# Kernel tuning notes

Hardware: AMD Instinct MI355X
Metric: run time of the kernel (lower is better)

## Reference

```python
import jax, jax.numpy as jnp
import numpy as np

SPATIAL = [(56, 100), (28, 50), (14, 25), (7, 13)]
L_TOT = sum(h * w for h, w in SPATIAL)  # 7441
IMG_H, IMG_W = 448.0, 800.0
HH, NLEV, NPTS = 8, 4, 4
C, FFN = 256, 1024
PC = [-54.0, -54.0, -5.0, 54.0, 54.0, 3.0]
GRID_XY = 1080 // 8


def mlp2(x, w1, b1, w2, b2):
    return jnp.maximum(x @ w1 + b1, 0.0) @ w2 + b2


def ln(x):
    m = x.mean(-1, keepdims=True)
    v = ((x - m) ** 2).mean(-1, keepdims=True)
    return (x - m) * jax.lax.rsqrt(v + 1e-5)


def bilinear_sample(feat, loc):
    # feat [h,w,D]; loc [N,2] normalized to [0,1]; zero padding, align_corners=False
    h, w = feat.shape[0], feat.shape[1]
    x = loc[:, 0] * w - 0.5
    y = loc[:, 1] * h - 0.5
    x0f = jnp.floor(x); y0f = jnp.floor(y)
    wx = (x - x0f)[:, None]; wy = (y - y0f)[:, None]
    x0 = x0f.astype(jnp.int32); y0 = y0f.astype(jnp.int32)
    def g(xi, yi):
        inb = ((xi >= 0) & (xi < w) & (yi >= 0) & (yi < h))[:, None]
        return feat[jnp.clip(yi, 0, h - 1), jnp.clip(xi, 0, w - 1)] * inb
    return (g(x0, y0) * (1 - wx) * (1 - wy) + g(x0 + 1, y0) * wx * (1 - wy)
            + g(x0, y0 + 1) * (1 - wx) * wy + g(x0 + 1, y0 + 1) * wx * wy)


def setup_inputs() -> dict:
    key = jax.random.key(0)
    ks = jax.random.split(key, 40)
    B, V, P = 4, 6, 200
    f = jnp.float32
    def w(i, shape, s=0.05):
        return jax.random.normal(ks[i], shape, f) * s
    inp = {
        'img_query_feat': jax.random.normal(ks[1], (B, C, P), f),
        'img_query_pos': jax.random.uniform(ks[2], (B, P, 3), dtype=f),
        'img_query_view_mask': jax.random.randint(ks[3], (B, P, V), 0, 2).astype(jnp.int32),
        'img_feats_stack': jax.random.normal(ks[4], (B, V, C, L_TOT), f),
        'normal_img_feats_pos_stack': jax.random.normal(ks[5], (L_TOT, 2), f),
        'lidar2img_rt': jnp.eye(4, dtype=f) + 0.01 * jax.random.normal(ks[0], (B, V, 4, 4), f),
        'lidar2cam_r': jnp.broadcast_to(jnp.eye(3, dtype=f), (B, V, 3, 3)) + 0.01 * jax.random.normal(ks[6], (B, V, 3, 3), f),
        'lidar2cam_t': jax.random.normal(ks[7], (B, V, 3), f),
        'qpos_w1': w(8, (3, C)), 'qpos_b1': jnp.zeros((C,), f),
        'qpos_w2': w(9, (C, C)), 'qpos_b2': jnp.zeros((C,), f),
        'kpos_w1': w(10, (6, C)), 'kpos_b1': jnp.zeros((C,), f),
        'kpos_w2': w(11, (C, C)), 'kpos_b2': jnp.zeros((C,), f),
        'sa_wq': w(12, (C, C)), 'sa_wk': w(13, (C, C)),
        'sa_wv': w(14, (C, C)), 'sa_wo': w(15, (C, C)),
        'dv_w': w(16, (C, C)),
        'doff_w': w(17, (C, HH * NLEV * NPTS * 2)), 'doff_b': jnp.zeros((HH * NLEV * NPTS * 2,), f),
        'dattn_w': w(18, (C, HH * NLEV * NPTS)), 'dattn_b': jnp.zeros((HH * NLEV * NPTS,), f),
        'dout_w': w(19, (C, C)),
        'ffn_w1': w(20, (C, FFN)), 'ffn_b1': jnp.zeros((FFN,), f),
        'ffn_w2': w(21, (FFN, C)), 'ffn_b2': jnp.zeros((C,), f),
        'pred_w1': w(22, (C, C)), 'pred_b1': jnp.zeros((C,), f),
        'pred_w2': w(23, (C, 3)), 'pred_b2': jnp.zeros((3,), f),
    }
    return inp


def reference(img_query_feat, img_query_pos, img_query_view_mask, img_feats_stack,
              normal_img_feats_pos_stack, lidar2img_rt, lidar2cam_r, lidar2cam_t,
              qpos_w1, qpos_b1, qpos_w2, qpos_b2, kpos_w1, kpos_b1, kpos_w2, kpos_b2,
              sa_wq, sa_wk, sa_wv, sa_wo, dv_w, doff_w, doff_b, dattn_w, dattn_b, dout_w,
              ffn_w1, ffn_b1, ffn_w2, ffn_b2, pred_w1, pred_b1, pred_w2, pred_b2):
    B, V, _, L = img_feats_stack.shape
    P = img_query_feat.shape[-1]
    Dh = C // HH

    # key 3D positions: denormalize -> backproject via inv(lidar2img) -> append cam center
    pos2d = jax.nn.sigmoid(normal_img_feats_pos_stack) * jnp.array([IMG_W, IMG_H], jnp.float32)
    pos4 = jnp.concatenate([pos2d, jnp.ones((L, 2), pos2d.dtype)], -1)  # [L,4]
    inv_rt = jnp.linalg.inv(lidar2img_rt)                               # [B,V,4,4]
    key3d = jnp.einsum('bvij,lj->bvli', inv_rt, pos4)[..., :3]          # [B,V,L,3]
    cam_t = -jnp.einsum('bvji,bvj->bvi', lidar2cam_r, lidar2cam_t)      # [B,V,3]
    key_pos6 = jnp.concatenate([key3d, jnp.broadcast_to(cam_t[:, :, None], key3d.shape)], -1)
    kpos_emb = mlp2(key_pos6, kpos_w1, kpos_b1, kpos_w2, kpos_b2)       # [B,V,L,C]
    qpos_emb = mlp2(img_query_pos, qpos_w1, qpos_b1, qpos_w2, qpos_b2)  # [B,P,C]

    # per-view normalized reference points from lidar->image projection
    qpad = jnp.concatenate([img_query_pos, jnp.ones((B, P, 1), img_query_pos.dtype)], -1)
    proj = jnp.einsum('bvij,bpj->bvpi', lidar2img_rt, qpad)
    ref = (proj[..., :2] / proj[..., 2:3]) / jnp.array([IMG_W, IMG_H], jnp.float32)  # [B,V,P,2]

    # on-image mask; views with <=1 query are skipped (as in original)
    mv = jnp.transpose(img_query_view_mask > 0, (0, 2, 1))  # [B,V,P]
    mv = mv & (mv.sum(-1, keepdims=True) > 1)

    # self attention among on-image queries (shared qkv, per-view key mask)
    x = jnp.transpose(img_query_feat, (0, 2, 1))  # [B,P,C]
    xq = x + qpos_emb
    q = (xq @ sa_wq).reshape(B, P, HH, Dh)
    k = (xq @ sa_wk).reshape(B, P, HH, Dh)
    v = (x @ sa_wv).reshape(B, P, HH, Dh)
    logits = jnp.einsum('bqhd,bkhd->bhqk', q, k) / np.sqrt(Dh).astype(np.float32)
    logits = logits[:, None] + jnp.where(mv[:, :, None, None, :], 0.0, -1e9)  # [B,V,HH,P,P]
    attn = jax.nn.softmax(logits, axis=-1)
    sa = jnp.einsum('bvhqk,bkhd->bvqhd', attn, v).reshape(B, V, P, C) @ sa_wo
    x1 = ln(x[:, None] + sa)  # [B,V,P,C]

    # multi-scale deformable cross attention
    vals = ((jnp.transpose(img_feats_stack, (0, 1, 3, 2)) + kpos_emb) @ dv_w).reshape(B, V, L, HH, Dh)
    q2 = x1 + qpos_emb[:, None]
    off = (q2 @ doff_w + doff_b).reshape(B, V, P, HH, NLEV, NPTS, 2)
    aw = jax.nn.softmax((q2 @ dattn_w + dattn_b).reshape(B, V, P, HH, NLEV * NPTS), -1)
    aw = aw.reshape(B, V, P, HH, NLEV, NPTS)
    wh = jnp.array([[float(w_), float(h_)] for (h_, w_) in SPATIAL], jnp.float32)  # [NLEV,2]
    loc = ref[:, :, :, None, None, None, :] + off / wh[:, None, :]
    out = jnp.zeros((B, V, P, HH, Dh), x.dtype)
    start = 0
    for l, (h_, w_) in enumerate(SPATIAL):
        feat_l = vals[:, :, start:start + h_ * w_]
        start += h_ * w_
        feat_l = jnp.transpose(feat_l.reshape(B, V, h_, w_, HH, Dh), (0, 1, 4, 2, 3, 5)).reshape(B * V * HH, h_, w_, Dh)
        loc_l = jnp.transpose(loc[:, :, :, :, l], (0, 1, 3, 2, 4, 5)).reshape(B * V * HH, P * NPTS, 2)
        s = jax.vmap(bilinear_sample)(feat_l, loc_l).reshape(B, V, HH, P, NPTS, Dh)
        out = out + jnp.einsum('bvhpnd,bvphn->bvphd', s, aw[:, :, :, :, l])
    x2 = ln(x1 + out.reshape(B, V, P, C) @ dout_w)
    x3 = ln(x2 + mlp2(x2, ffn_w1, ffn_b1, ffn_w2, ffn_b2))  # [B,V,P,C]

    # masked scatter-accumulate across views, count-normalized
    mk = mv[..., None].astype(x.dtype)            # [B,V,P,1]
    fused = (x3 * mk).sum(1) / (mk.sum(1) + 1e-4)  # [B,P,C]
    img_query_feat_out = jnp.transpose(fused, (0, 2, 1))

    # prediction head: center refinement + BEV normalization
    center = mlp2(fused, pred_w1, pred_b1, pred_w2, pred_b2) + img_query_pos  # [B,P,3]
    img_query_pos_out = jax.lax.stop_gradient(center)
    cx = (center[..., 0] - PC[0]) / (PC[3] - PC[0]) * GRID_XY
    cy = (center[..., 1] - PC[1]) / (PC[4] - PC[1]) * GRID_XY
    center_bev = jnp.stack([cx, cy], -1)
    img_query_pos_bev = jax.lax.stop_gradient(center_bev)
    height = jnp.transpose(center[..., 2:3], (0, 2, 1))
    center_out = jnp.transpose(center_bev, (0, 2, 1))
    return img_query_feat_out, img_query_pos_out, img_query_pos_bev, center_out, height
```

## Files before the change

### kernel.cpp

```cpp
#include <hip/hip_runtime.h>
#include <hip/hip_bf16.h>
#include <cstdint>
#include <cstddef>

using bf16 = __hip_bfloat16;
#define DEVFN static __device__ __forceinline__

constexpr int B = 4, V = 6, P = 200, C = 256, HH = 8, Dh = 32, NLEV = 4, NPTS = 4, FFN = 1024;
constexpr int L = 7441;
constexpr int BV = B * V, BP = B * P, BVP = B * V * P, BVL = B * V * L;
constexpr float IMG_W = 800.f, IMG_H = 448.f;

__constant__ int cLH[4] = {56, 28, 14, 7};
__constant__ int cLW[4] = {100, 50, 25, 13};
__constant__ int cLS[4] = {0, 5600, 7000, 7350};

constexpr size_t IRT   = 0;
constexpr size_t CAMT  = IRT + (size_t)BV * 16;
constexpr size_t MFLAG = CAMT + (size_t)BV * 3;
constexpr size_t Xo    = MFLAG + BV;
constexpr size_t QPOSo = Xo + (size_t)BP * C;
constexpr size_t Qo    = QPOSo + (size_t)BP * C;
constexpr size_t Ko    = Qo + (size_t)BP * C;
constexpr size_t VVo   = Ko + (size_t)BP * C;
constexpr size_t LOGo  = VVo + (size_t)BP * C;
constexpr size_t SAo   = LOGo + (size_t)B * HH * P * P;
constexpr size_t X1o   = SAo + (size_t)BVP * C;
constexpr size_t REFo  = X1o + (size_t)BVP * C;
constexpr size_t OFFo  = REFo + (size_t)BVP * 2;
constexpr size_t AWo   = OFFo + (size_t)BVP * 256;
constexpr size_t OUTSo = AWo + (size_t)BVP * 128;
constexpr size_t X2o   = OUTSo + (size_t)BVP * C;
constexpr size_t X3o   = X2o + (size_t)BVP * C;
constexpr size_t FUSEDo= X3o + (size_t)BVP * C;
constexpr size_t WS_FLOATS = FUSEDo + (size_t)BP * C;
constexpr size_t VALS_BYTE_OFF = ((WS_FLOATS * 4 + 255) / 256) * 256;
constexpr size_t VALS_ELEMS = (size_t)BVL * C;

constexpr size_t KW2T_O  = 0;
constexpr size_t DVWT_O  = 65536;
constexpr size_t WOT_O   = 131072;
constexpr size_t DOUTT_O = 196608;
constexpr size_t OAWT_O  = 262144;
constexpr size_t QKVT_O  = 360448;
constexpr size_t W1T_O   = 753664;
constexpr size_t W2T_O   = 1015808;
constexpr size_t HIDB_O  = 1277952;

constexpr size_t O0 = 0;
constexpr size_t O1 = O0 + (size_t)B * C * P;
constexpr size_t O2 = O1 + (size_t)B * P * 3;
constexpr size_t O3 = O2 + (size_t)B * P * 2;
constexpr size_t O4 = O3 + (size_t)B * 2 * P;

DEVFN float tof(bf16 x) { return __bfloat162float(x); }
DEVFN bf16  tobf(float x) { return __float2bfloat16(x); }

typedef __attribute__((ext_vector_type(8))) short short8;
typedef __attribute__((ext_vector_type(4))) float floatx4;

DEVFN float blockReduceSum(float v, float* red) {
    int j = threadIdx.x;
    __syncthreads();
    red[j] = v; __syncthreads();
    for (int s = 128; s > 0; s >>= 1) { if (j < s) red[j] += red[j + s]; __syncthreads(); }
    return red[0];
}

DEVFN float dotK(const float* __restrict__ s, const float* __restrict__ W, int j, int N, int K) {
    float acc = 0.f;
    for (int k = 0; k < K; k += 4) {
        float4 h = *(const float4*)(s + k);
        acc += h.x * W[(size_t)(k + 0) * N + j];
        acc += h.y * W[(size_t)(k + 1) * N + j];
        acc += h.z * W[(size_t)(k + 2) * N + j];
        acc += h.w * W[(size_t)(k + 3) * N + j];
    }
    return acc;
}

__global__ __launch_bounds__(64) void k_setup(const float* rt, const float* l2cr, const float* l2ct,
                                              const int* maskin, float* ws) {
    int t = threadIdx.x;
    if (t >= BV) return;
    float m[16], inv[16];
    for (int i = 0; i < 16; i++) m[i] = rt[t * 16 + i];
    inv[0]  =  m[5]*m[10]*m[15] - m[5]*m[11]*m[14] - m[9]*m[6]*m[15] + m[9]*m[7]*m[14] + m[13]*m[6]*m[11] - m[13]*m[7]*m[10];
    inv[4]  = -m[4]*m[10]*m[15] + m[4]*m[11]*m[14] + m[8]*m[6]*m[15] - m[8]*m[7]*m[14] - m[12]*m[6]*m[11] + m[12]*m[7]*m[10];
    inv[8]  =  m[4]*m[9]*m[15]  - m[4]*m[11]*m[13] - m[8]*m[5]*m[15] + m[8]*m[7]*m[13] + m[12]*m[5]*m[11] - m[12]*m[7]*m[9];
    inv[12] = -m[4]*m[9]*m[14]  + m[4]*m[10]*m[13] + m[8]*m[5]*m[14] - m[8]*m[6]*m[13] - m[12]*m[5]*m[10] + m[12]*m[6]*m[9];
    inv[1]  = -m[1]*m[10]*m[15] + m[1]*m[11]*m[14] + m[9]*m[2]*m[15] - m[9]*m[3]*m[14] - m[13]*m[2]*m[11] + m[13]*m[3]*m[10];
    inv[5]  =  m[0]*m[10]*m[15] - m[0]*m[11]*m[14] - m[8]*m[2]*m[15] + m[8]*m[3]*m[14] + m[12]*m[2]*m[11] - m[12]*m[3]*m[10];
    inv[9]  = -m[0]*m[9]*m[15]  + m[0]*m[11]*m[13] + m[8]*m[1]*m[15] - m[8]*m[3]*m[13] - m[12]*m[1]*m[11] + m[12]*m[3]*m[9];
    inv[13] =  m[0]*m[9]*m[14]  - m[0]*m[10]*m[13] - m[8]*m[1]*m[14] + m[8]*m[2]*m[13] + m[12]*m[1]*m[10] - m[12]*m[2]*m[9];
    inv[2]  =  m[1]*m[6]*m[15]  - m[1]*m[7]*m[14]  - m[5]*m[2]*m[15] + m[5]*m[3]*m[14] + m[13]*m[2]*m[7]  - m[13]*m[3]*m[6];
    inv[6]  = -m[0]*m[6]*m[15]  + m[0]*m[7]*m[14]  + m[4]*m[2]*m[15] - m[4]*m[3]*m[14] - m[12]*m[2]*m[7]  + m[12]*m[3]*m[6];
    inv[10] =  m[0]*m[5]*m[15]  - m[0]*m[7]*m[13]  - m[4]*m[1]*m[15] + m[4]*m[3]*m[13] + m[12]*m[1]*m[7]  - m[12]*m[3]*m[5];
    inv[14] = -m[0]*m[5]*m[14]  + m[0]*m[6]*m[13]  + m[4]*m[1]*m[14] - m[4]*m[2]*m[13] - m[12]*m[1]*m[6]  + m[12]*m[2]*m[5];
    inv[3]  = -m[1]*m[6]*m[11]  + m[1]*m[7]*m[10]  + m[5]*m[2]*m[11] - m[5]*m[3]*m[10] - m[9]*m[2]*m[7]   + m[9]*m[3]*m[6];
    inv[7]  =  m[0]*m[6]*m[11]  - m[0]*m[7]*m[10]  - m[4]*m[2]*m[11] + m[4]*m[3]*m[10] + m[8]*m[2]*m[7]   - m[8]*m[3]*m[6];
    inv[11] = -m[0]*m[5]*m[11]  + m[0]*m[7]*m[9]   + m[4]*m[1]*m[11] - m[4]*m[3]*m[9]  - m[8]*m[1]*m[7]   + m[8]*m[3]*m[5];
    inv[15] =  m[0]*m[5]*m[10]  - m[0]*m[6]*m[9]   - m[4]*m[1]*m[10] + m[4]*m[2]*m[9]  + m[8]*m[1]*m[6]   - m[8]*m[2]*m[5];
    float det = m[0]*inv[0] + m[1]*inv[4] + m[2]*inv[8] + m[3]*inv[12];
    float rd = 1.f / det;
    for (int i = 0; i < 16; i++) ws[IRT + t * 16 + i] = inv[i] * rd;
    float r9[9], tv[3];
    for (int i = 0; i < 9; i++) r9[i] = l2cr[t * 9 + i];
    for (int i = 0; i < 3; i++) tv[i] = l2ct[t * 3 + i];
    for (int i = 0; i < 3; i++)
        ws[CAMT + t * 3 + i] = -(r9[0 * 3 + i] * tv[0] + r9[1 * 3 + i] * tv[1] + r9[2 * 3 + i] * tv[2]);
    int b = t / V, v = t % V, cnt = 0;
    for (int p = 0; p < P; p++) cnt += (maskin[(b * P + p) * V + v] > 0) ? 1 : 0;
    ws[MFLAG + t] = (cnt > 1) ? 1.f : 0.f;
}

__global__ __launch_bounds__(256) void k_wprep_all(
        const float* kw2, const float* dvw, const float* wo, const float* dw,
        const float* offw, const float* attw, const float* wq, const float* wk, const float* wv,
        const float* w1, const float* w2, bf16* wb) {
    int bid = blockIdx.x, t = threadIdx.x;
    if (bid < 1024) {
        int reg = bid >> 8, n = bid & 255;
        const float* src = (reg == 0) ? kw2 : (reg == 1) ? dvw : (reg == 2) ? wo : dw;
        wb[(size_t)reg * 65536 + (size_t)n * 256 + t] = tobf(src[(size_t)t * 256 + n]);
    } else if (bid < 1408) {
        int n = bid - 1024;
        float v = (n < 256) ? offw[(size_t)t * 256 + n] : attw[(size_t)t * 128 + (n - 256)];
        wb[OAWT_O + (size_t)n * 256 + t] = tobf(v);
    } else if (bid < 2176) {
        int n = bid - 1408;
        bf16* dst = wb + QKVT_O + (size_t)n * 512;
        float v0 = (n < 256) ? wq[(size_t)t * 256 + n] : (n < 512) ? wk[(size_t)t * 256 + (n - 256)]
                                                                   : wv[(size_t)t * 256 + (n - 512)];
        dst[t] = tobf(v0);
        float v1 = (n < 256) ? wq[(size_t)t * 256 + n] : (n < 512) ? wk[(size_t)t * 256 + (n - 256)] : 0.f;
        dst[t + 256] = tobf(v1);
    } else if (bid < 3200) {
        int n = bid - 2176;
        wb[W1T_O + (size_t)n * 256 + t] = tobf(w1[(size_t)t * 1024 + n]);
    } else {
        int n = bid - 3200;
        bf16* dst = wb + W2T_O + (size_t)n * 1024;
        for (int kk = 0; kk < 4; kk++)
            dst[t + kk * 256] = tobf(w2[(size_t)(t + kk * 256) * 256 + n]);
    }
}

__global__ __launch_bounds__(256) void k_qpos(const float* qfeat, const float* qposin,
                                              const float* w1, const float* b1, const float* w2, const float* b2,
                                              float* ws) {
    int row = blockIdx.x, j = threadIdx.x;
    int b = row / P, p = row % P;
    __shared__ __align__(16) float pos[4];
    __shared__ __align__(16) float hid[C];
    if (j < 3) pos[j] = qposin[row * 3 + j];
    __syncthreads();
    float h = b1[j] + pos[0] * w1[0 * C + j] + pos[1] * w1[1 * C + j] + pos[2] * w1[2 * C + j];
    hid[j] = fmaxf(h, 0.f);
    __syncthreads();
    float acc = b2[j] + dotK(hid, w2, j, C, C);
    ws[QPOSo + (size_t)row * C + j] = acc;
    ws[Xo + (size_t)row * C + j] = qfeat[((size_t)b * C + j) * P + p];
}

constexpr int AST2 = 520;
__global__ __launch_bounds__(256) void k_qkv_mfma(const bf16* __restrict__ qkvT, float* ws) {
    __shared__ __align__(16) bf16 As[16 * AST2];
    int row0 = blockIdx.x * 16;
    int t = threadIdx.x;
    for (int rr = 0; rr < 16; rr++) {
        As[rr * AST2 + t]       = tobf(ws[Xo + (size_t)(row0 + rr) * C + t]);
        As[rr * AST2 + 256 + t] = tobf(ws[QPOSo + (size_t)(row0 + rr) * C + t]);
    }
    __syncthreads();
    int wave = t >> 6, lane = t & 63, quad = lane >> 4, l15 = lane & 15;
    int n0 = wave * 192;
    floatx4 acc[12];
    #pragma unroll
    for (int nt = 0; nt < 12; nt++) acc[nt] = (floatx4){0.f, 0.f, 0.f, 0.f};
    for (int kk = 0; kk < 16; kk++) {
        short8 a = *(const short8*)&As[l15 * AST2 + kk * 32 + quad * 8];
        #pragma unroll
        for (int nt = 0; nt < 12; nt++) {
            short8 bf = *(const short8*)&qkvT[(size_t)(n0 + nt * 16 + l15) * 512 + kk * 32 + quad * 8];
            acc[nt] = __builtin_amdgcn_mfma_f32_16x16x32_bf16(a, bf, acc[nt], 0, 0, 0);
        }
    }
    #pragma unroll
    for (int nt = 0; nt < 12; nt++) {
        int n = n0 + nt * 16 + l15;
        int which = n >> 8, c = n & 255;
        size_t dst = (which == 0) ? Qo : (which == 1) ? Ko : VVo;
        int row = row0 + quad * 4;
        #pragma unroll
        for (int u = 0; u < 4; u++)
            ws[dst + (size_t)(row + u) * C + c] = acc[nt][u];
    }
}

__global__ __launch_bounds__(256) void k_logits(float* ws) {
    int bid = blockIdx.x;
    int qi = bid % P, h = (bid / P) % HH, b = bid / (P * HH);
    int j = threadIdx.x;
    __shared__ __align__(16) float qf[Dh];
    if (j < Dh) qf[j] = ws[Qo + ((size_t)(b * P + qi)) * C + h * Dh + j];
    __syncthreads();
    if (j < P) {
        const float* kp = ws + Ko + ((size_t)(b * P + j)) * C + h * Dh;
        float acc = 0.f;
        for (int d = 0; d < Dh; d += 4) {
            float4 kv = *(const float4*)(kp + d);
            float4 qv = *(const float4*)(qf + d);
            acc += kv.x * qv.x + kv.y * qv.y + kv.z * qv.z + kv.w * qv.w;
        }
        ws[LOGo + (size_t)bid * P + j] = acc * 0.17677669529663687f;
    }
}

__global__ __launch_bounds__(256) void k_sattn(const int* maskin, float* ws) {
    int bid = blockIdx.x;
    int qi = bid % P, h = (bid / P) % HH, v = (bid / (P * HH)) % V, b = bid / (P * HH * V);
    int j = threadIdx.x;
    __shared__ float attn[256];
    __shared__ float red[256];
    __shared__ float rw[8];
    float flag = ws[MFLAG + b * V + v];
    float val = -1e30f;
    if (j < P) {
        float lg = ws[LOGo + ((size_t)(b * HH + h) * P + qi) * P + j];
        bool mk = (flag > 0.5f) && (maskin[(b * P + j) * V + v] > 0);
        val = lg + (mk ? 0.f : -1e9f);
    }
    int wv = j >> 6;
    float m = val;
    #pragma unroll
    for (int off = 32; off > 0; off >>= 1) m = fmaxf(m, __shfl_xor(m, off, 64));
    if ((j & 63) == 0) rw[wv] = m;
    __syncthreads();
    m = fmaxf(fmaxf(rw[0], rw[1]), fmaxf(rw[2], rw[3]));
    float e = (j < P) ? __expf(val - m) : 0.f;
    float s = e;
    #pragma unroll
    for (int off = 32; off > 0; off >>= 1) s += __shfl_xor(s, off, 64);
    if ((j & 63) == 0) rw[4 + wv] = s;
    __syncthreads();
    s = (rw[4] + rw[5]) + (rw[6] + rw[7]);
    attn[j] = e / s;
    __syncthreads();
    int d = j & 31, c = j >> 5;
    const float* vvp = ws + VVo + (size_t)b * P * C + h * Dh + d;
    float acc = 0.f;
    for (int kk = c * 25; kk < c * 25 + 25; ++kk) acc += attn[kk] * vvp[(size_t)kk * C];
    red[j] = acc; __syncthreads();
    if (j < Dh) {
        float s2 = 0.f;
        for (int c2 = 0; c2 < 8; c2++) s2 += red[c2 * 32 + j];
        ws[SAo + ((size_t)((b * V + v) * P + qi)) * C + h * Dh + j] = s2;
    }
}

constexpr int GAST = 264;
constexpr int OST = 260;
__global__ __launch_bounds__(256) void k_lngemm(const bf16* __restrict__ WT,
        float* ws, size_t aOff, size_t residOff, int residMode, size_t dstOff) {
    __shared__ __align__(16) bf16 As[32 * GAST];
    __shared__ __align__(16) float Os[32 * OST];
    __shared__ float redw[4][8][2];
    __shared__ float mv[8][2];
    int row0 = blockIdx.x * 32;
    int t = threadIdx.x;
    for (int rr = 0; rr < 32; rr++)
        As[rr * GAST + t] = tobf(ws[aOff + (size_t)(row0 + rr) * C + t]);
    __syncthreads();
    int wave = t >> 6, lane = t & 63, quad = lane >> 4, l15 = lane & 15;
    int n0 = wave * 64;
    floatx4 acc[2][4];
    #pragma unroll
    for (int i = 0; i < 2; i++)
        #pragma unroll
        for (int nt = 0; nt < 4; nt++) acc[i][nt] = (floatx4){0.f, 0.f, 0.f, 0.f};
    for (int kk = 0; kk < 8; kk++) {
        short8 a0 = *(const short8*)&As[l15 * GAST + kk * 32 + quad * 8];
        short8 a1 = *(const short8*)&As[(16 + l15) * GAST + kk * 32 + quad * 8];
        #pragma unroll
        for (int nt = 0; nt < 4; nt++) {
            short8 bf = *(const short8*)&WT[(size_t)(n0 + nt * 16 + l15) * 256 + kk * 32 + quad * 8];
            acc[0][nt] = __builtin_amdgcn_mfma_f32_16x16x32_bf16(a0, bf, acc[0][nt], 0, 0, 0);
            acc[1][nt] = __builtin_amdgcn_mfma_f32_16x16x32_bf16(a1, bf, acc[1][nt], 0, 0, 0);
        }
    }
    #pragma unroll
    for (int i = 0; i < 2; i++)
        #pragma unroll
        for (int nt = 0; nt < 4; nt++) {
            int col = n0 + nt * 16 + l15;
            int rl = i * 16 + quad * 4;
            #pragma unroll
            for (int u = 0; u < 4; u++) Os[(rl + u) * OST + col] = acc[i][nt][u];
        }
    __syncthreads();
    int lane2 = t & 63, wv = t >> 6;
    for (int g = 0; g < 4; g++) {
        float rv[8];
        #pragma unroll
        for (int r = 0; r < 8; r++) {
            int grow = row0 + g * 8 + r;
            int ridx = residMode ? ((grow / (P * V)) * P + grow % P) : grow;
            rv[r] = Os[(g * 8 + r) * OST + t] + ws[residOff + (size_t)ridx * C + t];
        }
        #pragma unroll
        for (int r = 0; r < 8; r++) {
            float s = rv[r], q = rv[r] * rv[r];
            for (int off = 32; off > 0; off >>= 1) {
                s += __shfl_down(s, off, 64);
                q += __shfl_down(q, off, 64);
            }
            if (lane2 == 0) { redw[wv][r][0] = s; redw[wv][r][1] = q; }
        }
        __syncthreads();
        if (t < 8) {
            float s = redw[0][t][0] + redw[1][t][0] + redw[2][t][0] + redw[3][t][0];
            float q = redw[0][t][1] + redw[1][t][1] + redw[2][t][1] + redw[3][t][1];
            float mean = s * (1.f / C);
            float var = q * (1.f / C) - mean * mean;
            mv[t][0] = mean; mv[t][1] = rsqrtf(var + 1e-5f);
        }
        __syncthreads();
        #pragma unroll
        for (int r = 0; r < 8; r++) {
            int grow = row0 + g * 8 + r;
            ws[dstOff + (size_t)grow * C + t] = (rv[r] - mv[r][0]) * mv[r][1];
        }
        __syncthreads();
    }
}

__global__ __launch_bounds__(256) void k_ref(const float* qposin, const float* rt, float* ws) {
    int tid = blockIdx.x * 256 + threadIdx.x;
    if (tid >= BVP) return;
    int p = tid % P, v = (tid / P) % V, b = tid / (P * V);
    float p0 = qposin[(b * P + p) * 3 + 0];
    float p1 = qposin[(b * P + p) * 3 + 1];
    float p2 = qposin[(b * P + p) * 3 + 2];
    const float* m = rt + (size_t)(b * V + v) * 16;
    float pr[3];
    for (int i = 0; i < 3; i++)
        pr[i] = m[i * 4 + 0] * p0 + m[i * 4 + 1] * p1 + m[i * 4 + 2] * p2 + m[i * 4 + 3];
    ws[REFo + (size_t)tid * 2 + 0] = pr[0] / pr[2] / IMG_W;
    ws[REFo + (size_t)tid * 2 + 1] = pr[1] / pr[2] / IMG_H;
}

constexpr int OAWST = 392;
__global__ __launch_bounds__(256) void k_offaw_mfma(const bf16* __restrict__ oawT,
        const float* __restrict__ ob, const float* __restrict__ ab, float* ws) {
    __shared__ __align__(16) bf16 As[32 * GAST];
    __shared__ __align__(16) float Os[32 * OAWST];
    int row0 = blockIdx.x * 32;
    int t = threadIdx.x;
    for (int rr = 0; rr < 32; rr++) {
        int grow = row0 + rr;
        int ridx = (grow / (P * V)) * P + grow % P;
        As[rr * GAST + t] = tobf(ws[X1o + (size_t)grow * C + t] + ws[QPOSo + (size_t)ridx * C + t]);
    }
    __syncthreads();
    int wave = t >> 6, lane = t & 63, quad = lane >> 4, l15 = lane & 15;
    int n0 = wave * 96;
    floatx4 acc[2][6];
    #pragma unroll
    for (int i = 0; i < 2; i++)
        #pragma unroll
        for (int nt = 0; nt < 6; nt++) acc[i][nt] = (floatx4){0.f, 0.f, 0.f, 0.f};
    for (int kk = 0; kk < 8; kk++) {
        short8 a0 = *(const short8*)&As[l15 * GAST + kk * 32 + quad * 8];
        short8 a1 = *(const short8*)&As[(16 + l15) * GAST + kk * 32 + quad * 8];
        #pragma unroll
        for (int nt = 0; nt < 6; nt++) {
            short8 bf = *(const short8*)&oawT[(size_t)(n0 + nt * 16 + l15) * 256 + kk * 32 + quad * 8];
            acc[0][nt] = __builtin_amdgcn_mfma_f32_16x16x32_bf16(a0, bf, acc[0][nt], 0, 0, 0);
            acc[1][nt] = __builtin_amdgcn_mfma_f32_16x16x32_bf16(a1, bf, acc[1][nt], 0, 0, 0);
        }
    }
    #pragma unroll
    for (int i = 0; i < 2; i++)
        #pragma unroll
        for (int nt = 0; nt < 6; nt++) {
            int col = n0 + nt * 16 + l15;
            int rl = i * 16 + quad * 4;
            #pragma unroll
            for (int u = 0; u < 4; u++) Os[(rl + u) * OAWST + col] = acc[i][nt][u];
        }
    __syncthreads();
    float obv = ob[t];
    for (int r = 0; r < 32; r++)
        ws[OFFo + (size_t)(row0 + r) * 256 + t] = Os[r * OAWST + t] + obv;
    {
        int r = t >> 3, g = t & 7;
        const float* lg = &Os[r * OAWST + 256 + g * 16];
        float mx = -1e30f;
        #pragma unroll
        for (int i = 0; i < 16; i++) mx = fmaxf(mx, lg[i] + ab[g * 16 + i]);
        float s = 0.f;
        float ex[16];
        #pragma unroll
        for (int i = 0; i < 16; i++) { ex[i] = __expf(lg[i] + ab[g * 16 + i] - mx); s += ex[i]; }
        float rs = 1.f / s;
        #pragma unroll
        for (int i = 0; i < 16; i++)
            ws[AWo + (size_t)(row0 + r) * 128 + g * 16 + i] = ex[i] * rs;
    }
}

constexpr int VROWS = 64;
constexpr int ASTR = C + 8;
constexpr int NVT = (L + VROWS - 1) / VROWS;

__global__ __launch_bounds__(256, 4) void k_vals_mfma(
        const float* __restrict__ npos, const float* __restrict__ feats,
        const float* __restrict__ kw1, const float* __restrict__ kb1, const float* __restrict__ kb2,
        const bf16* __restrict__ kw2T, const bf16* __restrict__ dvwT,
        const float* __restrict__ ws, bf16* __restrict__ vals) {
    __shared__ __align__(16) bf16 As[VROWS * ASTR];
    __shared__ float kp6s[VROWS][8];
    __shared__ float kb2s[C];
    int bv = blockIdx.y;
    int l0 = blockIdx.x * VROWS;
    int t = threadIdx.x;
    kb2s[t] = kb2[t];
    if (t < VROWS) {
        int l = min(l0 + t, L - 1);
        float sx = 1.f / (1.f + __expf(-npos[l * 2 + 0])) * IMG_W;
        float sy = 1.f / (1.f + __expf(-npos[l * 2 + 1])) * IMG_H;
        const float* inv = ws + IRT + (size_t)bv * 16;
        #pragma unroll
        for (int i = 0; i < 3; i++)
            kp6s[t][i] = inv[i * 4 + 0] * sx + inv[i * 4 + 1] * sy + inv[i * 4 + 2] + inv[i * 4 + 3];
        #pragma unroll
        for (int i = 0; i < 3; i++) kp6s[t][3 + i] = ws[CAMT + (size_t)bv * 3 + i];
    }
    __syncthreads();
    {
        float w1j[6];
        #pragma unroll
        for (int i = 0; i < 6; i++) w1j[i] = kw1[i * C + t];
        float bb = kb1[t];
        for (int r = 0; r < VROWS; r++) {
            float h = bb;
            #pragma unroll
            for (int i = 0; i < 6; i++) h += kp6s[r][i] * w1j[i];
            As[r * ASTR + t] = tobf(fmaxf(h, 0.f));
        }
    }
    __syncthreads();
    int wave = t >> 6, lane = t & 63;
    int quad = lane >> 4, l15 = lane & 15;
    int mh = (wave >> 1) * 32;
    int nh = (wave & 1) * 128;
    floatx4 acc[2][8];
    #pragma unroll
    for (int i = 0; i < 2; i++)
        #pragma unroll
        for (int nt = 0; nt < 8; nt++) acc[i][nt] = (floatx4){0.f, 0.f, 0.f, 0.f};
    for (int kk = 0; kk < 8; kk++) {
        short8 a0 = *(const short8*)&As[(mh + l15) * ASTR + kk * 32 + quad * 8];
        short8 a1 = *(const short8*)&As[(mh + 16 + l15) * ASTR + kk * 32 + quad * 8];
        #pragma unroll
        for (int nt = 0; nt < 8; nt++) {
            short8 bfr = *(const short8*)&kw2T[(size_t)(nh + nt * 16 + l15) * C + kk * 32 + quad * 8];
            acc[0][nt] = __builtin_amdgcn_mfma_f32_16x16x32_bf16(a0, bfr, acc[0][nt], 0, 0, 0);
            acc[1][nt] = __builtin_amdgcn_mfma_f32_16x16x32_bf16(a1, bfr, acc[1][nt], 0, 0, 0);
        }
    }
    __syncthreads();
    if (l0 + VROWS <= L) {
        #pragma unroll
        for (int i = 0; i < 2; i++)
            #pragma unroll
            for (int nt = 0; nt < 8; nt++) {
                int c = nh + nt * 16 + l15;
                int rb = mh + i * 16 + quad * 4;
                float4 f = *(const float4*)&feats[((size_t)bv * C + c) * L + l0 + rb];
                float bias = kb2s[c];
                As[(rb + 0) * ASTR + c] = tobf(acc[i][nt][0] + bias + f.x);
                As[(rb + 1) * ASTR + c] = tobf(acc[i][nt][1] + bias + f.y);
                As[(rb + 2) * ASTR + c] = tobf(acc[i][nt][2] + bias + f.z);
                As[(rb + 3) * ASTR + c] = tobf(acc[i][nt][3] + bias + f.w);
            }
    } else {
        #pragma unroll
        for (int i = 0; i < 2; i++)
            #pragma unroll
            for (int nt = 0; nt < 8; nt++) {
                int c = nh + nt * 16 + l15;
                int rb = mh + i * 16 + quad * 4;
                size_t fbase = ((size_t)bv * C + c) * L + l0 + rb;
                float bias = kb2s[c];
                #pragma unroll
                for (int u = 0; u < 4; u++) {
                    float fv = (l0 + rb + u < L) ? feats[fbase + u] : 0.f;
                    As[(rb + u) * ASTR + c] = tobf(acc[i][nt][u] + bias + fv);
                }
            }
    }
    __syncthreads();
    #pragma unroll
    for (int i = 0; i < 2; i++)
        #pragma unroll
        for (int nt = 0; nt < 8; nt++) acc[i][nt] = (floatx4){0.f, 0.f, 0.f, 0.f};
    for (int kk = 0; kk < 8; kk++) {
        short8 a0 = *(const short8*)&As[(mh + l15) * ASTR + kk * 32 + quad * 8];
        short8 a1 = *(const short8*)&As[(mh + 16 + l15) * ASTR + kk * 32 + quad * 8];
        #pragma unroll
        for (int nt = 0; nt < 8; nt++) {
            short8 bfr = *(const short8*)&dvwT[(size_t)(nh + nt * 16 + l15) * C + kk * 32 + quad * 8];
            acc[0][nt] = __builtin_amdgcn_mfma_f32_16x16x32_bf16(a0, bfr, acc[0][nt], 0, 0, 0);
            acc[1][nt] = __builtin_amdgcn_mfma_f32_16x16x32_bf16(a1, bfr, acc[1][nt], 0, 0, 0);
        }
    }
    __syncthreads();
    #pragma unroll
    for (int i = 0; i < 2; i++) {
        #pragma unroll
        for (int nt = 0; nt < 8; nt++) {
            int c = nh + nt * 16 + l15;
            int rb = mh + i * 16 + quad * 4;
            #pragma unroll
            for (int u = 0; u < 4; u++)
                As[(rb + u) * ASTR + c] = tobf(acc[i][nt][u]);
        }
    }
    __syncthreads();
    #pragma unroll
    for (int pass = 0; pass < 8; pass++) {
        int row = pass * 8 + (t >> 5);
        int col = (t & 31) * 8;
        int l = l0 + row;
        if (l < L)
            *(int4*)&vals[((size_t)bv * L + l) * C + col] = *(const int4*)&As[row * ASTR + col];
    }
}

__global__ __launch_bounds__(256) void k_sample(const float* ws, const bf16* vals, float* wsmut) {
    int bid0 = blockIdx.x;
    int row = (bid0 & 7) * (BVP / 8) + (bid0 >> 3);
    int j = threadIdx.x;
    int h = j >> 5, d = j & 31;
    __shared__ float soff[256];
    __shared__ float sawL[128];
    __shared__ float sref[2];
    soff[j] = ws[OFFo + (size_t)row * 256 + j];
    if (j < 128) sawL[j] = ws[AWo + (size_t)row * 128 + j];
    if (j < 2) sref[j] = ws[REFo + (size_t)row * 2 + j];
    __syncthreads();
    int v = (row / P) % V, b = row / (P * V);
    const bf16* vbase = vals + (size_t)(b * V + v) * L * C + h * Dh + d;
    float acc = 0.f;
    for (int l = 0; l < NLEV; l++) {
        float Wf = (float)cLW[l], Hf = (float)cLH[l];
        int Wi = cLW[l], Hi = cLH[l], S0 = cLS[l];
        for (int n = 0; n < NPTS; n++) {
            int oi = ((h * NLEV + l) * NPTS + n) * 2;
            float lx = sref[0] + soff[oi + 0] / Wf;
            float ly = sref[1] + soff[oi + 1] / Hf;
            float aww = sawL[(h * NLEV + l) * NPTS + n];
            float x = lx * Wf - 0.5f, y = ly * Hf - 0.5f;
            float x0f = floorf(x), y0f = floorf(y);
            float wx = x - x0f, wy = y - y0f;
            int x0 = (int)x0f, y0 = (int)y0f;
            float s = 0.f;
            #pragma unroll
            for (int dy = 0; dy < 2; dy++) {
                #pragma unroll
                for (int dx = 0; dx < 2; dx++) {
                    int xi = x0 + dx, yi = y0 + dy;
                    if (xi >= 0 && xi < Wi && yi >= 0 && yi < Hi) {
                        float wwt = (dx ? wx : 1.f - wx) * (dy ? wy : 1.f - wy);
                        s += wwt * tof(vbase[(size_t)(S0 + yi * Wi + xi) * C]);
                    }
                }
            }
            acc += aww * s;
        }
    }
    wsmut[OUTSo + (size_t)row * C + j] = acc;
}

__global__ __launch_bounds__(256) void k_ffn1(const bf16* __restrict__ w1T, const float* __restrict__ b1,
                                              float* ws, bf16* hidb) {
    __shared__ __align__(16) bf16 As[32 * GAST];
    __shared__ __align__(16) bf16 Hs[32 * AST2];
    int row0 = blockIdx.x * 32;
    int nb = blockIdx.y * 512;
    int t = threadIdx.x;
    for (int rr = 0; rr < 32; rr++)
        As[rr * GAST + t] = tobf(ws[X2o + (size_t)(row0 + rr) * C + t]);
    __syncthreads();
    int wave = t >> 6, lane = t & 63, quad = lane >> 4, l15 = lane & 15;
    int n0 = wave * 128;
    floatx4 acc[2][8];
    #pragma unroll
    for (int i = 0; i < 2; i++)
        #pragma unroll
        for (int nt = 0; nt < 8; nt++) acc[i][nt] = (floatx4){0.f, 0.f, 0.f, 0.f};
    for (int kk = 0; kk < 8; kk++) {
        short8 a0 = *(const short8*)&As[l15 * GAST + kk * 32 + quad * 8];
        short8 a1 = *(const short8*)&As[(16 + l15) * GAST + kk * 32 + quad * 8];
        #pragma unroll
        for (int nt = 0; nt < 8; nt++) {
            short8 bf = *(const short8*)&w1T[(size_t)(nb + n0 + nt * 16 + l15) * 256 + kk * 32 + quad * 8];
            acc[0][nt] = __builtin_amdgcn_mfma_f32_16x16x32_bf16(a0, bf, acc[0][nt], 0, 0, 0);
            acc[1][nt] = __builtin_amdgcn_mfma_f32_16x16x32_bf16(a1, bf, acc[1][nt], 0, 0, 0);
        }
    }
    #pragma unroll
    for (int i = 0; i < 2; i++)
        #pragma unroll
        for (int nt = 0; nt < 8; nt++) {
            int cl = n0 + nt * 16 + l15;
            float bias = b1[nb + cl];
            int rl = i * 16 + quad * 4;
            #pragma unroll
            for (int u = 0; u < 4; u++)
                Hs[(rl + u) * AST2 + cl] = tobf(fmaxf(acc[i][nt][u] + bias, 0.f));
        }
    __syncthreads();
    #pragma unroll
    for (int pass = 0; pass < 8; pass++) {
        int row = pass * 4 + (t >> 6);
        int col = (t & 63) * 8;
        *(int4*)&hidb[(size_t)(row0 + row) * FFN + nb + col] = *(const int4*)&Hs[row * AST2 + col];
    }
}

__global__ __launch_bounds__(256) void k_ffn2(const bf16* __restrict__ w2T, const float* __restrict__ b2,
                                              const bf16* __restrict__ hidb, float* ws) {
    __shared__ __align__(16) float Os[32 * OST];
    __shared__ float redw[4][8][2];
    __shared__ float mv[8][2];
    int row0 = blockIdx.x * 32;
    int t = threadIdx.x;
    int wave = t >> 6, lane = t & 63, quad = lane >> 4, l15 = lane & 15;
    int n0 = wave * 64;
    floatx4 acc[2][4];
    #pragma unroll
    for (int i = 0; i < 2; i++)
        #pragma unroll
        for (int nt = 0; nt < 4; nt++) acc[i][nt] = (floatx4){0.f, 0.f, 0.f, 0.f};
    for (int kk = 0; kk < 32; kk++) {
        short8 a0 = *(const short8*)&hidb[(size_t)(row0 + l15) * FFN + kk * 32 + quad * 8];
        short8 a1 = *(const short8*)&hidb[(size_t)(row0 + 16 + l15) * FFN + kk * 32 + quad * 8];
        #pragma unroll
        for (int nt = 0; nt < 4; nt++) {
            short8 bf = *(const short8*)&w2T[(size_t)(n0 + nt * 16 + l15) * FFN + kk * 32 + quad * 8];
            acc[0][nt] = __builtin_amdgcn_mfma_f32_16x16x32_bf16(a0, bf, acc[0][nt], 0, 0, 0);
            acc[1][nt] = __builtin_amdgcn_mfma_f32_16x16x32_bf16(a1, bf, acc[1][nt], 0, 0, 0);
        }
    }
    #pragma unroll
    for (int i = 0; i < 2; i++)
        #pragma unroll
        for (int nt = 0; nt < 4; nt++) {
            int col = n0 + nt * 16 + l15;
            float bias = b2[col];
            int rl = i * 16 + quad * 4;
            #pragma unroll
            for (int u = 0; u < 4; u++) Os[(rl + u) * OST + col] = acc[i][nt][u] + bias;
        }
    __syncthreads();
    for (int g = 0; g < 4; g++) {
        float rv[8];
        #pragma unroll
        for (int r = 0; r < 8; r++) {
            int grow = row0 + g * 8 + r;
            rv[r] = Os[(g * 8 + r) * OST + t] + ws[X2o + (size_t)grow * C + t];
        }
        #pragma unroll
        for (int r = 0; r < 8; r++) {
            float s = rv[r], q = rv[r] * rv[r];
            for (int off = 32; off > 0; off >>= 1) {
                s += __shfl_down(s, off, 64);
                q += __shfl_down(q, off, 64);
            }
            if (lane == 0) { redw[wave][r][0] = s; redw[wave][r][1] = q; }
        }
        __syncthreads();
        if (t < 8) {
            float s = redw[0][t][0] + redw[1][t][0] + redw[2][t][0] + redw[3][t][0];
            float q = redw[0][t][1] + redw[1][t][1] + redw[2][t][1] + redw[3][t][1];
            float mean = s * (1.f / C);
            float var = q * (1.f / C) - mean * mean;
            mv[t][0] = mean; mv[t][1] = rsqrtf(var + 1e-5f);
        }
        __syncthreads();
        #pragma unroll
        for (int r = 0; r < 8; r++) {
            int grow = row0 + g * 8 + r;
            ws[X3o + (size_t)grow * C + t] = (rv[r] - mv[r][0]) * mv[r][1];
        }
        __syncthreads();
    }
}

__global__ __launch_bounds__(256) void k_fuse(const int* maskin, float* ws, float* out) {
    int row = blockIdx.x, j = threadIdx.x;
    int b = row / P, p = row % P;
    float s = 0.f, cnt = 0.f;
    for (int v = 0; v < V; v++) {
        bool mk = (maskin[(b * P + p) * V + v] > 0) && (ws[MFLAG + b * V + v] > 0.5f);
        if (mk) {
            s += ws[X3o + ((size_t)((b * V + v) * P + p)) * C + j];
            cnt += 1.f;
        }
    }
    float f = s / (cnt + 1e-4f);
    ws[FUSEDo + (size_t)row * C + j] = f;
    out[O0 + ((size_t)b * C + j) * P + p] = f;
}

__global__ __launch_bounds__(256) void k_pred(const float* w1, const float* b1, const float* w2, const float* b2,
                                              const float* qposin, float* ws, float* out) {
    int row = blockIdx.x, j = threadIdx.x;
    __shared__ __align__(16) float in[C];
    __shared__ float red[256];
    __shared__ float cen[4];
    in[j] = ws[FUSEDo + (size_t)row * C + j];
    __syncthreads();
    float h = fmaxf(b1[j] + dotK(in, w1, j, C, C), 0.f);
    for (int i = 0; i < 3; i++) {
        float s = blockReduceSum(h * w2[j * 3 + i], red);
        if (j == 0) cen[i] = s + b2[i] + qposin[row * 3 + i];
    }
    if (j == 0) {
        float c0 = cen[0], c1 = cen[1], c2 = cen[2];
        float cx = (c0 + 54.f) / 108.f * 135.f;
        float cy = (c1 + 54.f) / 108.f * 135.f;
        int b = row / P, p = row % P;
        out[O1 + (size_t)row * 3 + 0] = c0;
        out[O1 + (size_t)row * 3 + 1] = c1;
        out[O1 + (size_t)row * 3 + 2] = c2;
        out[O2 + (size_t)row * 2 + 0] = cx;
        out[O2 + (size_t)row * 2 + 1] = cy;
        out[O3 + (size_t)b * 2 * P + 0 * P + p] = cx;
        out[O3 + (size_t)b * 2 * P + 1 * P + p] = cy;
        out[O4 + (size_t)b * P + p] = c2;
    }
}

extern "C" void kernel_launch(void* const* d_in, const int* in_sizes, int n_in,
                              void* d_out, int out_size, void* d_ws, size_t ws_size,
                              hipStream_t stream) {
    const float* qfeat  = (const float*)d_in[0];
    const float* qposin = (const float*)d_in[1];
    const int*   maskin = (const int*)d_in[2];
    const float* feats  = (const float*)d_in[3];
    const float* npos   = (const float*)d_in[4];
    const float* rt     = (const float*)d_in[5];
    const float* l2cr   = (const float*)d_in[6];
    const float* l2ct   = (const float*)d_in[7];
    const float* qp_w1 = (const float*)d_in[8],  * qp_b1 = (const float*)d_in[9];
    const float* qp_w2 = (const float*)d_in[10], * qp_b2 = (const float*)d_in[11];
    const float* kp_w1 = (const float*)d_in[12], * kp_b1 = (const float*)d_in[13];
    const float* kp_w2 = (const float*)d_in[14], * kp_b2 = (const float*)d_in[15];
    const float* sa_wq = (const float*)d_in[16], * sa_wk = (const float*)d_in[17];
    const float* sa_wv = (const float*)d_in[18], * sa_wv2 = nullptr;
    const float* sa_wo = (const float*)d_in[19];
    const float* dv_w  = (const float*)d_in[20];
    const float* doffw = (const float*)d_in[21], * doffb = (const float*)d_in[22];
    const float* dattw = (const float*)d_in[23], * dattb = (const float*)d_in[24];
    const float* doutw = (const float*)d_in[25];
    const float* f_w1  = (const float*)d_in[26], * f_b1 = (const float*)d_in[27];
    const float* f_w2  = (const float*)d_in[28], * f_b2 = (const float*)d_in[29];
    const float* p_w1  = (const float*)d_in[30], * p_b1 = (const float*)d_in[31];
    const float* p_w2  = (const float*)d_in[32], * p_b2 = (const float*)d_in[33];
    (void)sa_wv2;

    float* ws = (float*)d_ws;
    bf16* vals = (bf16*)((char*)d_ws + VALS_BYTE_OFF);
    bf16* wb = vals + VALS_ELEMS;
    bf16* hidb = wb + HIDB_O;
    float* out = (float*)d_out;

    k_setup<<<1, 64, 0, stream>>>(rt, l2cr, l2ct, maskin, ws);
    k_wprep_all<<<3456, 256, 0, stream>>>(kp_w2, dv_w, sa_wo, doutw, doffw, dattw,
                                          sa_wq, sa_wk, sa_wv, f_w1, f_w2, wb);
    k_qpos<<<BP, 256, 0, stream>>>(qfeat, qposin, qp_w1, qp_b1, qp_w2, qp_b2, ws);
    k_qkv_mfma<<<BP / 16, 256, 0, stream>>>(wb + QKVT_O, ws);
    k_logits<<<B * HH * P, 256, 0, stream>>>(ws);
    k_sattn<<<B * V * HH * P, 256, 0, stream>>>(maskin, ws);
    k_lngemm<<<BVP / 32, 256, 0, stream>>>(wb + WOT_O, ws, SAo, Xo, 1, X1o);
    k_ref<<<(BVP + 255) / 256, 256, 0, stream>>>(qposin, rt, ws);
    k_offaw_mfma<<<BVP / 32, 256, 0, stream>>>(wb + OAWT_O, doffb, dattb, ws);
    k_vals_mfma<<<dim3(NVT, BV), 256, 0, stream>>>(npos, feats, kp_w1, kp_b1, kp_b2,
                                                   wb + KW2T_O, wb + DVWT_O, ws, vals);
    k_sample<<<BVP, 256, 0, stream>>>(ws, vals, ws);
    k_lngemm<<<BVP / 32, 256, 0, stream>>>(wb + DOUTT_O, ws, OUTSo, X1o, 0, X2o);
    k_ffn1<<<dim3(BVP / 32, 2), 256, 0, stream>>>(wb + W1T_O, f_b1, ws, hidb);
    k_ffn2<<<BVP / 32, 256, 0, stream>>>(wb + W2T_O, f_b2, hidb, ws);
    k_fuse<<<BP, 256, 0, stream>>>(maskin, ws, out);
    k_pred<<<BP, 256, 0, stream>>>(p_w1, p_b1, p_w2, p_b2, qposin, ws, out);
}
```

Baseline: 883.3 us.

## Fold key-pos MLP second layer into value projection and prefetch features early

Precomputes a fused weight, kp_w2 times dv_w, plus a fused bias b2·dv_w in a new small kernel. This lets the value kernel accumulate relu(hidden)@fused and feats@dv_w into one accumulator, so the intermediate add-and-rewrite of the sum to shared memory is no longer needed. Feature loads are issued into registers before the first GEMM, so their global latency overlaps the MFMA work. Shared-memory indexing gets an XOR swizzle to reduce bank conflicts. In exchange, rounding the fused weight to bf16 changes numerics slightly, and the extra prefetch registers may lower occupancy.

```diff
diff --git a/kernel.cpp b/kernel.cpp
--- a/kernel.cpp
+++ b/kernel.cpp
@@ -33,11 +33,12 @@
 constexpr size_t X2o   = OUTSo + (size_t)BVP * C;
 constexpr size_t X3o   = X2o + (size_t)BVP * C;
 constexpr size_t FUSEDo= X3o + (size_t)BVP * C;
-constexpr size_t WS_FLOATS = FUSEDo + (size_t)BP * C;
+constexpr size_t B2DVo = FUSEDo + (size_t)BP * C;
+constexpr size_t WS_FLOATS = B2DVo + 256;
 constexpr size_t VALS_BYTE_OFF = ((WS_FLOATS * 4 + 255) / 256) * 256;
 constexpr size_t VALS_ELEMS = (size_t)BVL * C;
 
-constexpr size_t KW2T_O  = 0;
+constexpr size_t KW2NB_O = 0;
 constexpr size_t DVWT_O  = 65536;
 constexpr size_t WOT_O   = 131072;
 constexpr size_t DOUTT_O = 196608;
@@ -46,6 +47,7 @@
 constexpr size_t W1T_O   = 753664;
 constexpr size_t W2T_O   = 1015808;
 constexpr size_t HIDB_O  = 1277952;
+constexpr size_t KDVT_O  = HIDB_O;
 
 constexpr size_t O0 = 0;
 constexpr size_t O1 = O0 + (size_t)B * C * P;
@@ -121,8 +123,12 @@
     int bid = blockIdx.x, t = threadIdx.x;
     if (bid < 1024) {
         int reg = bid >> 8, n = bid & 255;
-        const float* src = (reg == 0) ? kw2 : (reg == 1) ? dvw : (reg == 2) ? wo : dw;
-        wb[(size_t)reg * 65536 + (size_t)n * 256 + t] = tobf(src[(size_t)t * 256 + n]);
+        if (reg == 0) {
+            wb[(size_t)n * 256 + t] = tobf(kw2[(size_t)n * 256 + t]);
+        } else {
+            const float* src = (reg == 1) ? dvw : (reg == 2) ? wo : dw;
+            wb[(size_t)reg * 65536 + (size_t)n * 256 + t] = tobf(src[(size_t)t * 256 + n]);
+        }
     } else if (bid < 1408) {
         int n = bid - 1024;
         float v = (n < 256) ? offw[(size_t)t * 256 + n] : attw[(size_t)t * 128 + (n - 256)];
@@ -146,6 +152,55 @@
     }
 }
 
+constexpr int GAST = 264;
+__global__ __launch_bounds__(256) void k_wfuse(const bf16* __restrict__ dvwT, const bf16* __restrict__ kw2nb,
+                                               const float* __restrict__ b2, bf16* __restrict__ kdvT,
+                                               float* ws) {
+    __shared__ __align__(16) bf16 As[32 * GAST];
+    int row0 = blockIdx.x * 32;
+    int t = threadIdx.x;
+    for (int rr = 0; rr < 32; rr++)
+        As[rr * GAST + t] = dvwT[(size_t)(row0 + rr) * 256 + t];
+    __syncthreads();
+    int wave = t >> 6, lane = t & 63, quad = lane >> 4, l15 = lane & 15;
+    int n0 = wave * 64;
+    floatx4 acc[2][4];
+    #pragma unroll
+    for (int i = 0; i < 2; i++)
+        #pragma unroll
+        for (int nt = 0; nt < 4; nt++) acc[i][nt] = (floatx4){0.f, 0.f, 0.f, 0.f};
+    for (int kk = 0; kk < 8; kk++) {
+        short8 a0 = *(const short8*)&As[l15 * GAST + kk * 32 + quad * 8];
+        short8 a1 = *(const short8*)&As[(16 + l15) * GAST + kk * 32 + quad * 8];
+        #pragma unroll
+        for (int nt = 0; nt < 4; nt++) {
+            short8 bf = *(const short8*)&kw2nb[(size_t)(n0 + nt * 16 + l15) * 256 + kk * 32 + quad * 8];
+            acc[0][nt] = __builtin_amdgcn_mfma_f32_16x16x32_bf16(a0, bf, acc[0][nt], 0, 0, 0);
+            acc[1][nt] = __builtin_amdgcn_mfma_f32_16x16x32_bf16(a1, bf, acc[1][nt], 0, 0, 0);
+        }
+    }
+    #pragma unroll
+    for (int i = 0; i < 2; i++)
+        #pragma unroll
+        for (int nt = 0; nt < 4; nt++) {
+            int col = n0 + nt * 16 + l15;
+            int rl = i * 16 + quad * 4;
+            #pragma unroll
+            for (int u = 0; u < 4; u++)
+                kdvT[(size_t)(row0 + rl + u) * 256 + col] = tobf(acc[i][nt][u]);
+        }
+    {
+        int r = t >> 3, pp = t & 7;
+        float s = 0.f;
+        for (int n = pp * 32; n < pp * 32 + 32; n++)
+            s += tof(As[r * GAST + n]) * b2[n];
+        s += __shfl_down(s, 4, 8);
+        s += __shfl_down(s, 2, 8);
+        s += __shfl_down(s, 1, 8);
+        if (pp == 0) ws[B2DVo + row0 + r] = s;
+    }
+}
+
 __global__ __launch_bounds__(256) void k_qpos(const float* qfeat, const float* qposin,
                                               const float* w1, const float* b1, const float* w2, const float* b2,
                                               float* ws) {
@@ -259,7 +314,6 @@
     }
 }
 
-constexpr int GAST = 264;
 constexpr int OST = 260;
 __global__ __launch_bounds__(256) void k_lngemm(const bf16* __restrict__ WT,
         float* ws, size_t aOff, size_t residOff, int residMode, size_t dstOff) {
@@ -414,18 +468,35 @@
 constexpr int ASTR = C + 8;
 constexpr int NVT = (L + VROWS - 1) / VROWS;
 
+DEVFN int swidx(int r, int c) {
+    return r * ASTR + ((c & 7) | ((((c >> 3) ^ ((r >> 3) & 7))) << 3));
+}
+DEVFN int swblk(int r, int cb) {
+    return r * ASTR + (((cb ^ ((r >> 3) & 7))) << 3);
+}
+
 __global__ __launch_bounds__(256, 4) void k_vals_mfma(
         const float* __restrict__ npos, const float* __restrict__ feats,
-        const float* __restrict__ kw1, const float* __restrict__ kb1, const float* __restrict__ kb2,
-        const bf16* __restrict__ kw2T, const bf16* __restrict__ dvwT,
+        const float* __restrict__ kw1, const float* __restrict__ kb1,
+        const bf16* __restrict__ kdvT, const bf16* __restrict__ dvwT,
         const float* __restrict__ ws, bf16* __restrict__ vals) {
     __shared__ __align__(16) bf16 As[VROWS * ASTR];
     __shared__ float kp6s[VROWS][8];
-    __shared__ float kb2s[C];
+    __shared__ float b2s[C];
     int bv = blockIdx.y;
     int l0 = blockIdx.x * VROWS;
     int t = threadIdx.x;
-    kb2s[t] = kb2[t];
+    bool full = (l0 + VROWS <= L);
+
+    float4 fb1[8];
+    if (full) {
+        #pragma unroll
+        for (int rnd = 0; rnd < 8; rnd++) {
+            int c = rnd * 16 + (t >> 4), ql = (t & 15) * 4;
+            fb1[rnd] = *(const float4*)&feats[((size_t)bv * C + c) * L + l0 + ql];
+        }
+    }
+    b2s[t] = ws[B2DVo + t];
     if (t < VROWS) {
         int l = min(l0 + t, L - 1);
         float sx = 1.f / (1.f + __expf(-npos[l * 2 + 0])) * IMG_W;
@@ -447,7 +518,7 @@
             float h = bb;
             #pragma unroll
             for (int i = 0; i < 6; i++) h += kp6s[r][i] * w1j[i];
-            As[r * ASTR + t] = tobf(fmaxf(h, 0.f));
+            As[swidx(r, t)] = tobf(fmaxf(h, 0.f));
         }
     }
     __syncthreads();
@@ -461,54 +532,54 @@
         #pragma unroll
         for (int nt = 0; nt < 8; nt++) acc[i][nt] = (floatx4){0.f, 0.f, 0.f, 0.f};
     for (int kk = 0; kk < 8; kk++) {
-        short8 a0 = *(const short8*)&As[(mh + l15) * ASTR + kk * 32 + quad * 8];
-        short8 a1 = *(const short8*)&As[(mh + 16 + l15) * ASTR + kk * 32 + quad * 8];
+        short8 a0 = *(const short8*)&As[swblk(mh + l15, kk * 4 + quad)];
+        short8 a1 = *(const short8*)&As[swblk(mh + 16 + l15, kk * 4 + quad)];
         #pragma unroll
         for (int nt = 0; nt < 8; nt++) {
-            short8 bfr = *(const short8*)&kw2T[(size_t)(nh + nt * 16 + l15) * C + kk * 32 + quad * 8];
+            short8 bfr = *(const short8*)&kdvT[(size_t)(nh + nt * 16 + l15) * C + kk * 32 + quad * 8];
             acc[0][nt] = __builtin_amdgcn_mfma_f32_16x16x32_bf16(a0, bfr, acc[0][nt], 0, 0, 0);
             acc[1][nt] = __builtin_amdgcn_mfma_f32_16x16x32_bf16(a1, bfr, acc[1][nt], 0, 0, 0);
         }
     }
     __syncthreads();
-    if (l0 + VROWS <= L) {
-        #pragma unroll
-        for (int i = 0; i < 2; i++)
+    if (full) {
+        float4 fb2[8];
+        #pragma unroll
+        for (int rnd = 0; rnd < 8; rnd++) {
+            int c = 128 + rnd * 16 + (t >> 4), ql = (t & 15) * 4;
+            fb2[rnd] = *(const float4*)&feats[((size_t)bv * C + c) * L + l0 + ql];
+        }
+        #pragma unroll
+        for (int rnd = 0; rnd < 8; rnd++) {
+            int c = rnd * 16 + (t >> 4), ql = (t & 15) * 4;
+            As[swidx(ql + 0, c)] = tobf(fb1[rnd].x);
+            As[swidx(ql + 1, c)] = tobf(fb1[rnd].y);
+            As[swidx(ql + 2, c)] = tobf(fb1[rnd].z);
+            As[swidx(ql + 3, c)] = tobf(fb1[rnd].w);
+        }
+        #pragma unroll
+        for (int rnd = 0; rnd < 8; rnd++) {
+            int c = 128 + rnd * 16 + (t >> 4), ql = (t & 15) * 4;
+            As[swidx(ql + 0, c)] = tobf(fb2[rnd].x);
+            As[swidx(ql + 1, c)] = tobf(fb2[rnd].y);
+            As[swidx(ql + 2, c)] = tobf(fb2[rnd].z);
+            As[swidx(ql + 3, c)] = tobf(fb2[rnd].w);
+        }
+    } else {
+        for (int rnd = 0; rnd < 16; rnd++) {
+            int c = rnd * 16 + (t >> 4), ql = (t & 15) * 4;
+            size_t fbase = ((size_t)bv * C + c) * L + l0 + ql;
             #pragma unroll
-            for (int nt = 0; nt < 8; nt++) {
-                int c = nh + nt * 16 + l15;
-                int rb = mh + i * 16 + quad * 4;
-                float4 f = *(const float4*)&feats[((size_t)bv * C + c) * L + l0 + rb];
-                float bias = kb2s[c];
-                As[(rb + 0) * ASTR + c] = tobf(acc[i][nt][0] + bias + f.x);
-                As[(rb + 1) * ASTR + c] = tobf(acc[i][nt][1] + bias + f.y);
-                As[(rb + 2) * ASTR + c] = tobf(acc[i][nt][2] + bias + f.z);
-                As[(rb + 3) * ASTR + c] = tobf(acc[i][nt][3] + bias + f.w);
+            for (int u = 0; u < 4; u++) {
+                float fv = (l0 + ql + u < L) ? feats[fbase + u] : 0.f;
+                As[swidx(ql + u, c)] = tobf(fv);
             }
-    } else {
-        #pragma unroll
-        for (int i = 0; i < 2; i++)
-            #pragma unroll
-            for (int nt = 0; nt < 8; nt++) {
-                int c = nh + nt * 16 + l15;
-                int rb = mh + i * 16 + quad * 4;
-                size_t fbase = ((size_t)bv * C + c) * L + l0 + rb;
-                float bias = kb2s[c];
-                #pragma unroll
-                for (int u = 0; u < 4; u++) {
-                    float fv = (l0 + rb + u < L) ? feats[fbase + u] : 0.f;
-                    As[(rb + u) * ASTR + c] = tobf(acc[i][nt][u] + bias + fv);
-                }
-            }
-    }
-    __syncthreads();
-    #pragma unroll
-    for (int i = 0; i < 2; i++)
-        #pragma unroll
-        for (int nt = 0; nt < 8; nt++) acc[i][nt] = (floatx4){0.f, 0.f, 0.f, 0.f};
+        }
+    }
+    __syncthreads();
     for (int kk = 0; kk < 8; kk++) {
-        short8 a0 = *(const short8*)&As[(mh + l15) * ASTR + kk * 32 + quad * 8];
-        short8 a1 = *(const short8*)&As[(mh + 16 + l15) * ASTR + kk * 32 + quad * 8];
+        short8 a0 = *(const short8*)&As[swblk(mh + l15, kk * 4 + quad)];
+        short8 a1 = *(const short8*)&As[swblk(mh + 16 + l15, kk * 4 + quad)];
         #pragma unroll
         for (int nt = 0; nt < 8; nt++) {
             short8 bfr = *(const short8*)&dvwT[(size_t)(nh + nt * 16 + l15) * C + kk * 32 + quad * 8];
@@ -523,19 +594,20 @@
         for (int nt = 0; nt < 8; nt++) {
             int c = nh + nt * 16 + l15;
             int rb = mh + i * 16 + quad * 4;
+            float bias = b2s[c];
             #pragma unroll
             for (int u = 0; u < 4; u++)
-                As[(rb + u) * ASTR + c] = tobf(acc[i][nt][u]);
+                As[swidx(rb + u, c)] = tobf(acc[i][nt][u] + bias);
         }
     }
     __syncthreads();
     #pragma unroll
     for (int pass = 0; pass < 8; pass++) {
         int row = pass * 8 + (t >> 5);
-        int col = (t & 31) * 8;
+        int cb = t & 31;
         int l = l0 + row;
         if (l < L)
-            *(int4*)&vals[((size_t)bv * L + l) * C + col] = *(const int4*)&As[row * ASTR + col];
+            *(int4*)&vals[((size_t)bv * L + l) * C + cb * 8] = *(const int4*)&As[swblk(row, cb)];
     }
 }
 
@@ -761,7 +833,7 @@
     const float* kp_w1 = (const float*)d_in[12], * kp_b1 = (const float*)d_in[13];
     const float* kp_w2 = (const float*)d_in[14], * kp_b2 = (const float*)d_in[15];
     const float* sa_wq = (const float*)d_in[16], * sa_wk = (const float*)d_in[17];
-    const float* sa_wv = (const float*)d_in[18], * sa_wv2 = nullptr;
+    const float* sa_wv = (const float*)d_in[18];
     const float* sa_wo = (const float*)d_in[19];
     const float* dv_w  = (const float*)d_in[20];
     const float* doffw = (const float*)d_in[21], * doffb = (const float*)d_in[22];
@@ -771,7 +843,6 @@
     const float* f_w2  = (const float*)d_in[28], * f_b2 = (const float*)d_in[29];
     const float* p_w1  = (const float*)d_in[30], * p_b1 = (const float*)d_in[31];
     const float* p_w2  = (const float*)d_in[32], * p_b2 = (const float*)d_in[33];
-    (void)sa_wv2;
 
     float* ws = (float*)d_ws;
     bf16* vals = (bf16*)((char*)d_ws + VALS_BYTE_OFF);
@@ -782,6 +853,7 @@
     k_setup<<<1, 64, 0, stream>>>(rt, l2cr, l2ct, maskin, ws);
     k_wprep_all<<<3456, 256, 0, stream>>>(kp_w2, dv_w, sa_wo, doutw, doffw, dattw,
                                           sa_wq, sa_wk, sa_wv, f_w1, f_w2, wb);
+    k_wfuse<<<8, 256, 0, stream>>>(wb + DVWT_O, wb + KW2NB_O, kp_b2, wb + KDVT_O, ws);
     k_qpos<<<BP, 256, 0, stream>>>(qfeat, qposin, qp_w1, qp_b1, qp_w2, qp_b2, ws);
     k_qkv_mfma<<<BP / 16, 256, 0, stream>>>(wb + QKVT_O, ws);
     k_logits<<<B * HH * P, 256, 0, stream>>>(ws);
@@ -789,8 +861,8 @@
     k_lngemm<<<BVP / 32, 256, 0, stream>>>(wb + WOT_O, ws, SAo, Xo, 1, X1o);
     k_ref<<<(BVP + 255) / 256, 256, 0, stream>>>(qposin, rt, ws);
     k_offaw_mfma<<<BVP / 32, 256, 0, stream>>>(wb + OAWT_O, doffb, dattb, ws);
-    k_vals_mfma<<<dim3(NVT, BV), 256, 0, stream>>>(npos, feats, kp_w1, kp_b1, kp_b2,
-                                                   wb + KW2T_O, wb + DVWT_O, ws, vals);
+    k_vals_mfma<<<dim3(NVT, BV), 256, 0, stream>>>(npos, feats, kp_w1, kp_b1,
+                                                   wb + KDVT_O, wb + DVWT_O, ws, vals);
     k_sample<<<BVP, 256, 0, stream>>>(ws, vals, ws);
     k_lngemm<<<BVP / 32, 256, 0, stream>>>(wb + DOUTT_O, ws, OUTSo, X1o, 0, X2o);
     k_ffn1<<<dim3(BVP / 32, 2), 256, 0, stream>>>(wb + W1T_O, f_b1, ws, hidb);
```

New measurement: 871.6 us. No clear change (-1.3%).
